# Kernel optimization log

Hardware: AMD Instinct MI355X
Metric: run time of the kernel (lower is better)

Reference implementation:

```python
import jax, jax.numpy as jnp
import numpy as np

E, D, H = 8, 2048, 2048  # num_experts, features, expert_dim
B, L, K = 2, 2048, 2


def setup_inputs() -> dict:
    key = jax.random.key(0)
    k1, k2, k3, k4, k5, k6 = jax.random.split(key, 6)
    x = jax.random.normal(k1, (B, L, D), dtype=jnp.float32)
    w = jax.random.uniform(k2, (B, L, K), dtype=jnp.float32)
    weights = w / jnp.sum(w, axis=-1, keepdims=True)  # normalised routing weights
    expert_indices = jax.random.randint(k3, (B, L, K), 0, E, dtype=jnp.int64)
    gate_up = jax.random.normal(k4, (E, D, 2 * H), dtype=jnp.float32) * 0.02
    down = jax.random.normal(k5, (E, H, D), dtype=jnp.float32) * 0.02
    per_expert_scale = 1.0 + 0.01 * jax.random.normal(k6, (E,), dtype=jnp.float32)
    return {"x": x, "weights": weights, "expert_indices": expert_indices,
            "gate_up": gate_up, "down": down, "per_expert_scale": per_expert_scale}


def reference(x, weights, expert_indices, gate_up, down, per_expert_scale):
    Bb, Ll, Dd = x.shape
    Ee = gate_up.shape[0]
    N = Bb * Ll
    xf = x.reshape(N, Dd)                                   # [N, D]
    idx = expert_indices.reshape(N, -1)                     # [N, K]
    wts = weights.reshape(N, -1)                            # [N, K]
    # combine[n, e] = sum_k weights[n,k] * 1[idx[n,k]==e]; scale folded in.
    onehot = jax.nn.one_hot(idx, Ee, dtype=x.dtype)         # [N, K, E]
    combine = jnp.einsum('nk,nke->ne', wts, onehot) * per_expert_scale  # [N, E]
    # Dense per-expert GatedMLP (grouped GEMM across all experts).
    h = jnp.einsum('nd,edh->enh', xf, gate_up)              # [E, N, 2H]
    gate, up = jnp.split(h, 2, axis=-1)
    act = jax.nn.gelu(gate, approximate=False) * up         # exact gelu, as torch F.gelu
    y = jnp.einsum('enh,ehd->end', act, down)               # [E, N, D]
    out = jnp.einsum('end,ne->nd', y, combine)              # weighted combine over experts
    return out.reshape(Bb, Ll, Dd)
```

## Files before the change

kernel.cpp:

```cpp
#include <hip/hip_runtime.h>
#include <math.h>

#define EXPERTS 8
#define DDIM 2048
#define HDIM 2048
#define NTOK 4096
#define NPAIR 8192
#define MAXSLOT 10240
#define MAXTILE 40

typedef _Float16 f16;
typedef __attribute__((ext_vector_type(8))) _Float16 f16x8;
typedef __attribute__((ext_vector_type(2))) _Float16 f16x2;
typedef __attribute__((ext_vector_type(4))) float f32x4;

#define GUPT_OFF 0ull
#define Y_OFF    0ull
#define DWNT_OFF 41943040ull
#define XF_OFF   134217728ull
#define ACT_OFF  150994944ull
#define CTRL_OFF 192937984ull
#define CTRL_INTS 28776

#define BARRIER() asm volatile("s_barrier" ::: "memory")
#define VMCNT3()  asm volatile("s_waitcnt vmcnt(3)" ::: "memory")
#define VMCNT2()  asm volatile("s_waitcnt vmcnt(2)" ::: "memory")
#define VMCNT0()  asm volatile("s_waitcnt vmcnt(0)" ::: "memory")

__device__ __forceinline__ void gload_lds16(const void* g, void* l) {
  __builtin_amdgcn_global_load_lds(
      (const __attribute__((address_space(1))) unsigned int*)g,
      (__attribute__((address_space(3))) unsigned int*)l,
      16, 0, 0);
}

__device__ __forceinline__ int swz(int r) { return (r + (r >> 2)) & 3; }

__global__ void k_detect(const int* __restrict__ w, int* flag) {
  int i = blockIdx.x * blockDim.x + threadIdx.x;
  if (i < NPAIR / 2 && w[2 * i + 1] != 0) atomicOr(flag, 1);
}

__device__ __forceinline__ int expert_of(const int* idx, int is32, int p) {
  return is32 ? idx[p] : idx[2 * p];
}

__global__ void k_count(const int* __restrict__ idx, const int* __restrict__ flag,
                        int* cnt) {
  int p = blockIdx.x * blockDim.x + threadIdx.x;
  if (p < NPAIR) atomicAdd(&cnt[expert_of(idx, *flag, p)], 1);
}

__global__ void k_plan(const int* __restrict__ cnt, int* cursor,
                       int* tile_e, int* tile_r0, int* n_tiles) {
  if (blockIdx.x == 0 && threadIdx.x == 0) {
    int off = 0, nt = 0;
    for (int e = 0; e < EXPERTS; ++e) {
      cursor[e] = off;
      int t = (cnt[e] + 255) >> 8;
      for (int i = 0; i < t; ++i) { tile_e[nt] = e; tile_r0[nt] = off + i * 256; ++nt; }
      off += t * 256;
    }
    *n_tiles = nt;
  }
}

__global__ void k_assign(const int* __restrict__ idx, const int* __restrict__ flag,
                         const float* __restrict__ wts, const float* __restrict__ scale,
                         int* cursor, int* slot_tok, int* tok_slot, float* slot_w) {
  int p = blockIdx.x * blockDim.x + threadIdx.x;
  if (p < NPAIR) {
    int e = expert_of(idx, *flag, p);
    int pos = atomicAdd(&cursor[e], 1);
    slot_tok[pos] = p >> 1;
    tok_slot[p] = pos;
    slot_w[pos] = wts[p] * scale[e];
  }
}

__global__ void k_cvt_x(const float* __restrict__ in, f16* __restrict__ out) {
  int i = blockIdx.x * blockDim.x + threadIdx.x;
  float4 v = ((const float4*)in)[i];
  typedef __attribute__((ext_vector_type(4))) _Float16 f16x4;
  f16x4 o = {(f16)v.x, (f16)v.y, (f16)v.z, (f16)v.w};
  ((f16x4*)out)[i] = o;
}

__global__ void k_transpose(const float* __restrict__ in, f16* __restrict__ out,
                            int R, int C) {
  __shared__ float t[32][33];
  const size_t base = (size_t)blockIdx.z * R * C;
  const float* ip = in + base;
  f16* op = out + base;
  int c0 = blockIdx.x * 32, r0 = blockIdx.y * 32;
  int tx = threadIdx.x, ty = threadIdx.y;
#pragma unroll
  for (int i = 0; i < 32; i += 8)
    t[ty + i][tx] = ip[(size_t)(r0 + ty + i) * C + c0 + tx];
  __syncthreads();
  const int p = tx & 15, h = tx >> 4;
#pragma unroll
  for (int i = 0; i < 2; ++i) {
    const int j = ty + h * 8 + i * 16;
    f16x2 v = {(f16)t[2 * p][j], (f16)t[2 * p + 1][j]};
    *(f16x2*)&op[(size_t)(c0 + j) * R + r0 + 2 * p] = v;
  }
}

template <int G1>
__global__ __launch_bounds__(512, 4) void k_gemm(
    const f16* __restrict__ Asrc, const f16* __restrict__ Bsrc,
    const int* __restrict__ slot_tok,
    const int* __restrict__ tile_e, const int* __restrict__ tile_r0,
    const int* __restrict__ n_tiles, f16* __restrict__ dst) {
  constexpr int NC = G1 ? 4 : 2;
  constexpr int BUFH = 8192 + (G1 ? 128 : 64) * 32;
  __shared__ __align__(16) f16 smem[3][BUFH];

  const int q = (MAXTILE * 32) / 8;
  int oid = (int)(blockIdx.y * MAXTILE + blockIdx.x);
  int nid = (oid & 7) * q + (oid >> 3);
  const int nt = nid & 31, bx = nid >> 5;
  if (bx >= *n_tiles) return;
  const int e = tile_e[bx];
  const int m0 = tile_r0[bx];

  const int tid = threadIdx.x;
  const int lane = tid & 63;
  const int wv = tid >> 6;
  const int wm = wv >> 1;
  const int wn = wv & 1;
  const int fr = lane & 15;
  const int fhi = lane >> 4;

  const int cc = tid & 3;
  const int ar0 = tid >> 2;
  const f16* aS[2];
#pragma unroll
  for (int i = 0; i < 2; ++i) {
    const int rl = i * 128 + ar0;
    size_t arow = G1 ? (size_t)slot_tok[m0 + rl] : (size_t)(m0 + rl);
    aS[i] = Asrc + arow * 2048 + (cc ^ swz(rl)) * 8;
  }
  const f16* bS = nullptr;
  if (G1 || tid < 256) {
    const int rb = tid >> 2;
    size_t brow;
    if (G1) brow = (size_t)e * 4096 + (rb < 64 ? (size_t)(nt * 64 + rb)
                                               : (size_t)(2048 + nt * 64 + rb - 64));
    else    brow = (size_t)e * 2048 + nt * 64 + rb;
    bS = Bsrc + brow * 2048 + (cc ^ swz(rb)) * 8;
  }

  auto stage = [&](int s, int kt) {
    const size_t ko = (size_t)kt * 32;
    gload_lds16(aS[0] + ko, &smem[s][tid * 8]);
    gload_lds16(aS[1] + ko, &smem[s][4096 + tid * 8]);
    if (G1 || tid < 256) gload_lds16(bS + ko, &smem[s][8192 + tid * 8]);
  };

  f32x4 acc[4][NC];
#pragma unroll
  for (int i = 0; i < 4; ++i)
#pragma unroll
    for (int j = 0; j < NC; ++j) acc[i][j] = (f32x4){0.f, 0.f, 0.f, 0.f};

  stage(0, 0);
  stage(1, 1);
  if (G1 || wv < 4) { VMCNT3(); } else { VMCNT2(); }
  BARRIER();

  const int NT = 64;
  int s = 0;
  for (int kt = 0; kt < NT; ++kt) {
    int s2 = (s == 0) ? 2 : s - 1;
    if (kt + 2 < NT) stage(s2, kt + 2);

    const f16* As = &smem[s][0];
    const f16* Bs = &smem[s][8192];
    f16x8 af[4];
#pragma unroll
    for (int mi = 0; mi < 4; ++mi) {
      const int r = wm * 64 + mi * 16 + fr;
      af[mi] = *(const f16x8*)&As[r * 32 + ((fhi ^ swz(r)) << 3)];
    }
#pragma unroll
    for (int ci = 0; ci < NC; ++ci) {
      int rb;
      if (G1) rb = (ci < 2 ? 0 : 64) + (wn * 2 + (ci & 1)) * 16 + fr;
      else    rb = (wn * 2 + ci) * 16 + fr;
      const f16x8 b = *(const f16x8*)&Bs[rb * 32 + ((fhi ^ swz(rb)) << 3)];
#pragma unroll
      for (int mi = 0; mi < 4; ++mi)
        acc[mi][ci] = __builtin_amdgcn_mfma_f32_16x16x32_f16(af[mi], b,
                                                             acc[mi][ci], 0, 0, 0);
    }
    if (kt + 1 < NT) {
      if (kt + 2 < NT) { if (G1 || wv < 4) { VMCNT3(); } else { VMCNT2(); } }
      else { VMCNT0(); }
      BARRIER();
    }
    s = (s == 2) ? 0 : s + 1;
  }

  if (G1) {
#pragma unroll
    for (int mi = 0; mi < 4; ++mi)
#pragma unroll
      for (int ci = 0; ci < 2; ++ci)
#pragma unroll
        for (int rg = 0; rg < 4; ++rg) {
          const int row = m0 + wm * 64 + mi * 16 + fhi * 4 + rg;
          const int col = nt * 64 + (wn * 2 + ci) * 16 + fr;
          const float g = acc[mi][ci][rg];
          const float u = acc[mi][ci + 2][rg];
          const float a = 0.5f * g * (1.0f + erff(g * 0.70710678118654752f)) * u;
          dst[(size_t)row * 2048 + col] = (f16)a;
        }
  } else {
#pragma unroll
    for (int mi = 0; mi < 4; ++mi)
#pragma unroll
      for (int ci = 0; ci < 2; ++ci)
#pragma unroll
        for (int rg = 0; rg < 4; ++rg)
          dst[(size_t)(m0 + wm * 64 + mi * 16 + fhi * 4 + rg) * 2048 +
              nt * 64 + (wn * 2 + ci) * 16 + fr] = (f16)acc[mi][ci][rg];
  }
}

__global__ void k_combine(const f16* __restrict__ y, const float* __restrict__ slot_w,
                          const int* __restrict__ tok_slot, float* __restrict__ out) {
  const int gid = blockIdx.x * blockDim.x + threadIdx.x;
  const int tok = gid >> 8;
  const int c = (gid & 255) * 8;
  const int s0 = tok_slot[2 * tok], s1 = tok_slot[2 * tok + 1];
  const float w0 = slot_w[s0], w1 = slot_w[s1];
  const f16x8 v0 = *(const f16x8*)&y[(size_t)s0 * 2048 + c];
  const f16x8 v1 = *(const f16x8*)&y[(size_t)s1 * 2048 + c];
  float o[8];
#pragma unroll
  for (int j = 0; j < 8; ++j) o[j] = w0 * (float)v0[j] + w1 * (float)v1[j];
  float4* op = (float4*)&out[(size_t)tok * 2048 + c];
  op[0] = (float4){o[0], o[1], o[2], o[3]};
  op[1] = (float4){o[4], o[5], o[6], o[7]};
}

extern "C" void kernel_launch(void* const* d_in, const int* in_sizes, int n_in,
                              void* d_out, int out_size, void* d_ws, size_t ws_size,
                              hipStream_t stream) {
  const float* x = (const float*)d_in[0];
  const float* wts = (const float*)d_in[1];
  const int* idx = (const int*)d_in[2];
  const float* gup = (const float*)d_in[3];
  const float* dwn = (const float*)d_in[4];
  const float* scale = (const float*)d_in[5];
  float* out = (float*)d_out;

  char* ws = (char*)d_ws;
  f16* gup_t = (f16*)(ws + GUPT_OFF);
  f16* y = (f16*)(ws + Y_OFF);
  f16* down_t = (f16*)(ws + DWNT_OFF);
  f16* xf = (f16*)(ws + XF_OFF);
  f16* act = (f16*)(ws + ACT_OFF);
  int* ctrl = (int*)(ws + CTRL_OFF);
  int* slot_tok = ctrl;
  int* tok_slot = ctrl + 10240;
  int* cnt = ctrl + 18432;
  int* cursor = ctrl + 18440;
  int* tile_e = ctrl + 18448;
  int* tile_r0 = ctrl + 18488;
  int* n_tiles = ctrl + 18528;
  int* is32 = ctrl + 18529;
  float* slot_w = (float*)(ctrl + 18536);

  hipMemsetAsync(ctrl, 0, (size_t)CTRL_INTS * sizeof(int), stream);

  k_detect<<<NPAIR / 2 / 256, 256, 0, stream>>>(idx, is32);
  k_count<<<NPAIR / 256, 256, 0, stream>>>(idx, is32, cnt);
  k_plan<<<1, 1, 0, stream>>>(cnt, cursor, tile_e, tile_r0, n_tiles);
  k_assign<<<NPAIR / 256, 256, 0, stream>>>(idx, is32, wts, scale, cursor,
                                            slot_tok, tok_slot, slot_w);
  k_cvt_x<<<NTOK * DDIM / 4 / 256, 256, 0, stream>>>(x, xf);
  k_transpose<<<dim3(4096 / 32, 2048 / 32, EXPERTS), dim3(32, 8), 0, stream>>>(
      gup, gup_t, 2048, 4096);
  k_gemm<1><<<dim3(MAXTILE, 32), 512, 0, stream>>>(xf, gup_t, slot_tok, tile_e,
                                                   tile_r0, n_tiles, act);
  k_transpose<<<dim3(2048 / 32, 2048 / 32, EXPERTS), dim3(32, 8), 0, stream>>>(
      dwn, down_t, 2048, 2048);
  k_gemm<0><<<dim3(MAXTILE, 32), 512, 0, stream>>>(act, down_t, slot_tok, tile_e,
                                                   tile_r0, n_tiles, y);
  k_combine<<<NTOK, 256, 0, stream>>>(y, slot_w, tok_slot, out);
}
```

Measured before the change: 551.2 us.

## Fuse fp32 weight transpose-convert into GEMM B-loads and shrink token tiles

Removes the two separate transpose/convert kernels. Each GEMM now reads the fp32 expert weights directly, converts them to f16 in registers and writes them transposed into LDS, which cuts a full extra read and write of both weight tensors. Token tiles shrink from 256 to 128 rows, so less padding is wasted per expert. The workgroup drops to 256 threads with double buffering and setprio around the MFMA block. In exchange, the B operand now uses register-staged loads of twice the bytes, and every M-tile re-reads the fp32 weights, which adds memory traffic per tile.

```diff
diff --git a/kernel.cpp b/kernel.cpp
--- a/kernel.cpp
+++ b/kernel.cpp
@@ -6,26 +6,23 @@
 #define HDIM 2048
 #define NTOK 4096
 #define NPAIR 8192
-#define MAXSLOT 10240
-#define MAXTILE 40
+#define MAXSLOT 9216
+#define MAXTILE 72
 
 typedef _Float16 f16;
 typedef __attribute__((ext_vector_type(8))) _Float16 f16x8;
-typedef __attribute__((ext_vector_type(2))) _Float16 f16x2;
+typedef __attribute__((ext_vector_type(4))) _Float16 f16x4;
 typedef __attribute__((ext_vector_type(4))) float f32x4;
 
-#define GUPT_OFF 0ull
-#define Y_OFF    0ull
-#define DWNT_OFF 41943040ull
-#define XF_OFF   134217728ull
-#define ACT_OFF  150994944ull
-#define CTRL_OFF 192937984ull
-#define CTRL_INTS 28776
+#define XF_OFF   0ull
+#define ACT_OFF  16777216ull
+#define Y_OFF    54525952ull
+#define CTRL_OFF 92274688ull
+#define CTRL_INTS 26792
 
 #define BARRIER() asm volatile("s_barrier" ::: "memory")
-#define VMCNT3()  asm volatile("s_waitcnt vmcnt(3)" ::: "memory")
-#define VMCNT2()  asm volatile("s_waitcnt vmcnt(2)" ::: "memory")
-#define VMCNT0()  asm volatile("s_waitcnt vmcnt(0)" ::: "memory")
+#define VMCNT(n)  asm volatile("s_waitcnt vmcnt(" #n ")" ::: "memory")
+#define LGKM0()   asm volatile("s_waitcnt lgkmcnt(0)" ::: "memory")
 
 __device__ __forceinline__ void gload_lds16(const void* g, void* l) {
   __builtin_amdgcn_global_load_lds(
@@ -34,7 +31,7 @@
       16, 0, 0);
 }
 
-__device__ __forceinline__ int swz(int r) { return (r + (r >> 2)) & 3; }
+__device__ __forceinline__ int swz(int r) { return (r >> 1) & 3; }
 
 __global__ void k_detect(const int* __restrict__ w, int* flag) {
   int i = blockIdx.x * blockDim.x + threadIdx.x;
@@ -57,9 +54,9 @@
     int off = 0, nt = 0;
     for (int e = 0; e < EXPERTS; ++e) {
       cursor[e] = off;
-      int t = (cnt[e] + 255) >> 8;
-      for (int i = 0; i < t; ++i) { tile_e[nt] = e; tile_r0[nt] = off + i * 256; ++nt; }
-      off += t * 256;
+      int t = (cnt[e] + 127) >> 7;
+      for (int i = 0; i < t; ++i) { tile_e[nt] = e; tile_r0[nt] = off + i * 128; ++nt; }
+      off += t * 128;
     }
     *n_tiles = nt;
   }
@@ -81,49 +78,24 @@
 __global__ void k_cvt_x(const float* __restrict__ in, f16* __restrict__ out) {
   int i = blockIdx.x * blockDim.x + threadIdx.x;
   float4 v = ((const float4*)in)[i];
-  typedef __attribute__((ext_vector_type(4))) _Float16 f16x4;
   f16x4 o = {(f16)v.x, (f16)v.y, (f16)v.z, (f16)v.w};
   ((f16x4*)out)[i] = o;
 }
 
-__global__ void k_transpose(const float* __restrict__ in, f16* __restrict__ out,
-                            int R, int C) {
-  __shared__ float t[32][33];
-  const size_t base = (size_t)blockIdx.z * R * C;
-  const float* ip = in + base;
-  f16* op = out + base;
-  int c0 = blockIdx.x * 32, r0 = blockIdx.y * 32;
-  int tx = threadIdx.x, ty = threadIdx.y;
-#pragma unroll
-  for (int i = 0; i < 32; i += 8)
-    t[ty + i][tx] = ip[(size_t)(r0 + ty + i) * C + c0 + tx];
-  __syncthreads();
-  const int p = tx & 15, h = tx >> 4;
-#pragma unroll
-  for (int i = 0; i < 2; ++i) {
-    const int j = ty + h * 8 + i * 16;
-    f16x2 v = {(f16)t[2 * p][j], (f16)t[2 * p + 1][j]};
-    *(f16x2*)&op[(size_t)(c0 + j) * R + r0 + 2 * p] = v;
-  }
-}
-
 template <int G1>
-__global__ __launch_bounds__(512, 4) void k_gemm(
-    const f16* __restrict__ Asrc, const f16* __restrict__ Bsrc,
+__global__ __launch_bounds__(256, 3) void k_gemm(
+    const f16* __restrict__ Asrc, const float* __restrict__ W,
     const int* __restrict__ slot_tok,
     const int* __restrict__ tile_e, const int* __restrict__ tile_r0,
     const int* __restrict__ n_tiles, f16* __restrict__ dst) {
-  constexpr int NC = G1 ? 4 : 2;
-  constexpr int BUFH = 8192 + (G1 ? 128 : 64) * 32;
-  __shared__ __align__(16) f16 smem[3][BUFH];
-
-  const int q = (MAXTILE * 32) / 8;
-  int oid = (int)(blockIdx.y * MAXTILE + blockIdx.x);
-  int nid = (oid & 7) * q + (oid >> 3);
-  const int nt = nid & 31, bx = nid >> 5;
+  __shared__ __align__(16) f16 smem[2][8192];
+
+  const int bx = blockIdx.y;
   if (bx >= *n_tiles) return;
+  const int nt = blockIdx.x;
   const int e = tile_e[bx];
   const int m0 = tile_r0[bx];
+  const int LDB = G1 ? 4096 : 2048;
 
   const int tid = threadIdx.x;
   const int lane = tid & 63;
@@ -133,74 +105,109 @@
   const int fr = lane & 15;
   const int fhi = lane >> 4;
 
-  const int cc = tid & 3;
-  const int ar0 = tid >> 2;
   const f16* aS[2];
 #pragma unroll
   for (int i = 0; i < 2; ++i) {
-    const int rl = i * 128 + ar0;
-    size_t arow = G1 ? (size_t)slot_tok[m0 + rl] : (size_t)(m0 + rl);
-    aS[i] = Asrc + arow * 2048 + (cc ^ swz(rl)) * 8;
-  }
-  const f16* bS = nullptr;
-  if (G1 || tid < 256) {
-    const int rb = tid >> 2;
-    size_t brow;
-    if (G1) brow = (size_t)e * 4096 + (rb < 64 ? (size_t)(nt * 64 + rb)
-                                               : (size_t)(2048 + nt * 64 + rb - 64));
-    else    brow = (size_t)e * 2048 + nt * 64 + rb;
-    bS = Bsrc + brow * 2048 + (cc ^ swz(rb)) * 8;
-  }
-
-  auto stage = [&](int s, int kt) {
-    const size_t ko = (size_t)kt * 32;
-    gload_lds16(aS[0] + ko, &smem[s][tid * 8]);
-    gload_lds16(aS[1] + ko, &smem[s][4096 + tid * 8]);
-    if (G1 || tid < 256) gload_lds16(bS + ko, &smem[s][8192 + tid * 8]);
+    const int r = i * 64 + (tid >> 2);
+    size_t arow = G1 ? (size_t)slot_tok[m0 + r] : (size_t)(m0 + r);
+    aS[i] = Asrc + arow * 2048 + ((tid & 3) ^ swz(r)) * 8;
+  }
+  auto gloadA = [&](int s, int kt) {
+#pragma unroll
+    for (int i = 0; i < 2; ++i)
+      gload_lds16(aS[i] + (size_t)kt * 32, &smem[s][i * 2048 + tid * 8]);
   };
 
-  f32x4 acc[4][NC];
+  const int cp = tid & 63;
+  const int kf = tid >> 6;
+  int gcol;
+  if (G1) gcol = (cp < 32) ? nt * 64 + 2 * cp : 2048 + nt * 64 + (2 * cp - 64);
+  else    gcol = nt * 128 + 2 * cp;
+  const float* bP = W + (size_t)e * 2048 * LDB + (size_t)(8 * kf) * LDB + gcol;
+  const int bbase = 2 * cp * 32 + ((kf ^ (cp & 3)) << 3);
+
+  float2 q0, q1, q2, q3, q4, q5, q6, q7;
+  auto loadB = [&](int kt) {
+    const float* p = bP + (size_t)kt * 32 * LDB;
+    q0 = *(const float2*)(p);
+    q1 = *(const float2*)(p + LDB);
+    q2 = *(const float2*)(p + 2 * LDB);
+    q3 = *(const float2*)(p + 3 * LDB);
+    q4 = *(const float2*)(p + 4 * LDB);
+    q5 = *(const float2*)(p + 5 * LDB);
+    q6 = *(const float2*)(p + 6 * LDB);
+    q7 = *(const float2*)(p + 7 * LDB);
+  };
+  auto writeB = [&](int s) {
+    f16x8 wa = {(f16)q0.x, (f16)q1.x, (f16)q2.x, (f16)q3.x,
+                (f16)q4.x, (f16)q5.x, (f16)q6.x, (f16)q7.x};
+    f16x8 wb = {(f16)q0.y, (f16)q1.y, (f16)q2.y, (f16)q3.y,
+                (f16)q4.y, (f16)q5.y, (f16)q6.y, (f16)q7.y};
+    f16* B = &smem[s][4096];
+    *(f16x8*)&B[bbase] = wa;
+    *(f16x8*)&B[bbase + 32] = wb;
+  };
+
+  int ctv[4];
+#pragma unroll
+  for (int ci = 0; ci < 4; ++ci) {
+    if (G1) ctv[ci] = (ci < 2) ? (wn * 2 + ci) : (4 + wn * 2 + (ci - 2));
+    else    ctv[ci] = wn * 4 + ci;
+  }
+
+  f32x4 acc[4][4];
 #pragma unroll
   for (int i = 0; i < 4; ++i)
 #pragma unroll
-    for (int j = 0; j < NC; ++j) acc[i][j] = (f32x4){0.f, 0.f, 0.f, 0.f};
-
-  stage(0, 0);
-  stage(1, 1);
-  if (G1 || wv < 4) { VMCNT3(); } else { VMCNT2(); }
+    for (int j = 0; j < 4; ++j) acc[i][j] = (f32x4){0.f, 0.f, 0.f, 0.f};
+
+  loadB(0);
+  gloadA(0, 0);
+  VMCNT(2);
+  writeB(0);
+  loadB(1);
+  VMCNT(8);
+  LGKM0();
   BARRIER();
 
   const int NT = 64;
-  int s = 0;
   for (int kt = 0; kt < NT; ++kt) {
-    int s2 = (s == 0) ? 2 : s - 1;
-    if (kt + 2 < NT) stage(s2, kt + 2);
+    const int s = kt & 1;
+    if (kt + 1 < NT) {
+      gloadA(s ^ 1, kt + 1);
+      VMCNT(2);
+      writeB(s ^ 1);
+    }
+    if (kt + 2 < NT) loadB(kt + 2);
 
     const f16* As = &smem[s][0];
-    const f16* Bs = &smem[s][8192];
-    f16x8 af[4];
+    const f16* Bs = &smem[s][4096];
+    f16x8 af[4], bf[4];
 #pragma unroll
     for (int mi = 0; mi < 4; ++mi) {
       const int r = wm * 64 + mi * 16 + fr;
       af[mi] = *(const f16x8*)&As[r * 32 + ((fhi ^ swz(r)) << 3)];
     }
 #pragma unroll
-    for (int ci = 0; ci < NC; ++ci) {
-      int rb;
-      if (G1) rb = (ci < 2 ? 0 : 64) + (wn * 2 + (ci & 1)) * 16 + fr;
-      else    rb = (wn * 2 + ci) * 16 + fr;
-      const f16x8 b = *(const f16x8*)&Bs[rb * 32 + ((fhi ^ swz(rb)) << 3)];
-#pragma unroll
-      for (int mi = 0; mi < 4; ++mi)
-        acc[mi][ci] = __builtin_amdgcn_mfma_f32_16x16x32_f16(af[mi], b,
+    for (int ci = 0; ci < 4; ++ci) {
+      const int c = ctv[ci] * 16 + fr;
+      bf[ci] = *(const f16x8*)&Bs[c * 32 + ((fhi ^ swz(c)) << 3)];
+    }
+    __builtin_amdgcn_s_setprio(1);
+#pragma unroll
+    for (int mi = 0; mi < 4; ++mi)
+#pragma unroll
+      for (int ci = 0; ci < 4; ++ci)
+        acc[mi][ci] = __builtin_amdgcn_mfma_f32_16x16x32_f16(af[mi], bf[ci],
                                                              acc[mi][ci], 0, 0, 0);
-    }
+    __builtin_amdgcn_s_setprio(0);
+
     if (kt + 1 < NT) {
-      if (kt + 2 < NT) { if (G1 || wv < 4) { VMCNT3(); } else { VMCNT2(); } }
-      else { VMCNT0(); }
+      if (kt + 2 < NT) { VMCNT(8); }
+      else { VMCNT(0); }
+      LGKM0();
       BARRIER();
     }
-    s = (s == 2) ? 0 : s + 1;
   }
 
   if (G1) {
@@ -221,11 +228,13 @@
 #pragma unroll
     for (int mi = 0; mi < 4; ++mi)
 #pragma unroll
-      for (int ci = 0; ci < 2; ++ci)
-#pragma unroll
-        for (int rg = 0; rg < 4; ++rg)
-          dst[(size_t)(m0 + wm * 64 + mi * 16 + fhi * 4 + rg) * 2048 +
-              nt * 64 + (wn * 2 + ci) * 16 + fr] = (f16)acc[mi][ci][rg];
+      for (int ci = 0; ci < 4; ++ci)
+#pragma unroll
+        for (int rg = 0; rg < 4; ++rg) {
+          const int row = m0 + wm * 64 + mi * 16 + fhi * 4 + rg;
+          const int col = nt * 128 + wn * 64 + ci * 16 + fr;
+          dst[(size_t)row * 2048 + col] = (f16)acc[mi][ci][rg];
+        }
   }
 }
 
@@ -258,21 +267,19 @@
   float* out = (float*)d_out;
 
   char* ws = (char*)d_ws;
-  f16* gup_t = (f16*)(ws + GUPT_OFF);
-  f16* y = (f16*)(ws + Y_OFF);
-  f16* down_t = (f16*)(ws + DWNT_OFF);
   f16* xf = (f16*)(ws + XF_OFF);
   f16* act = (f16*)(ws + ACT_OFF);
+  f16* y = (f16*)(ws + Y_OFF);
   int* ctrl = (int*)(ws + CTRL_OFF);
   int* slot_tok = ctrl;
-  int* tok_slot = ctrl + 10240;
-  int* cnt = ctrl + 18432;
-  int* cursor = ctrl + 18440;
-  int* tile_e = ctrl + 18448;
-  int* tile_r0 = ctrl + 18488;
-  int* n_tiles = ctrl + 18528;
-  int* is32 = ctrl + 18529;
-  float* slot_w = (float*)(ctrl + 18536);
+  int* tok_slot = ctrl + 9216;
+  int* cnt = ctrl + 17408;
+  int* cursor = ctrl + 17416;
+  int* tile_e = ctrl + 17424;
+  int* tile_r0 = ctrl + 17496;
+  int* n_tiles = ctrl + 17568;
+  int* is32 = ctrl + 17569;
+  float* slot_w = (float*)(ctrl + 17576);
 
   hipMemsetAsync(ctrl, 0, (size_t)CTRL_INTS * sizeof(int), stream);
 
@@ -282,13 +289,9 @@
   k_assign<<<NPAIR / 256, 256, 0, stream>>>(idx, is32, wts, scale, cursor,
                                             slot_tok, tok_slot, slot_w);
   k_cvt_x<<<NTOK * DDIM / 4 / 256, 256, 0, stream>>>(x, xf);
-  k_transpose<<<dim3(4096 / 32, 2048 / 32, EXPERTS), dim3(32, 8), 0, stream>>>(
-      gup, gup_t, 2048, 4096);
-  k_gemm<1><<<dim3(MAXTILE, 32), 512, 0, stream>>>(xf, gup_t, slot_tok, tile_e,
+  k_gemm<1><<<dim3(32, MAXTILE), 256, 0, stream>>>(xf, gup, slot_tok, tile_e,
                                                    tile_r0, n_tiles, act);
-  k_transpose<<<dim3(2048 / 32, 2048 / 32, EXPERTS), dim3(32, 8), 0, stream>>>(
-      dwn, down_t, 2048, 2048);
-  k_gemm<0><<<dim3(MAXTILE, 32), 512, 0, stream>>>(act, down_t, slot_tok, tile_e,
+  k_gemm<0><<<dim3(16, MAXTILE), 256, 0, stream>>>(act, dwn, slot_tok, tile_e,
                                                    tile_r0, n_tiles, y);
   k_combine<<<NTOK, 256, 0, stream>>>(y, slot_w, tok_slot, out);
 }
```

Measured after the change: 517.4 us. -6.1%, faster.
